# Optimization experiments

Hardware: AMD Instinct MI355X
Metric: run time of the kernel (lower is better)

The kernel has to match this reference:

```python
import jax, jax.numpy as jnp
import numpy as np

K_CONST = 0.005
D_U = 0.001
D_V = 0.005
LAYERS = [3, 256, 256, 256, 256, 2]
N_PTS = 131072


def setup_inputs() -> dict:
    key = jax.random.key(0)
    ks = jax.random.split(key, 3 + 2 * (len(LAYERS) - 1))
    inp = {
        "t": jax.random.uniform(ks[0], (N_PTS, 1), dtype=jnp.float32),
        "x": jax.random.uniform(ks[1], (N_PTS, 1), dtype=jnp.float32),
        "y": jax.random.uniform(ks[2], (N_PTS, 1), dtype=jnp.float32),
    }
    # PyTorch nn.Linear default init: U(-1/sqrt(fan_in), 1/sqrt(fan_in))
    for i in range(len(LAYERS) - 1):
        fan_in = LAYERS[i]
        s = 1.0 / np.sqrt(fan_in)
        inp[f"W{i}"] = jax.random.uniform(ks[3 + 2 * i], (LAYERS[i], LAYERS[i + 1]),
                                          minval=-s, maxval=s, dtype=jnp.float32)
        inp[f"b{i}"] = jax.random.uniform(ks[4 + 2 * i], (LAYERS[i + 1],),
                                          minval=-s, maxval=s, dtype=jnp.float32)
    return inp


def _mlp(params, inp):
    # inp: (3,) -> (2,) tanh MLP (tanh on all but last layer)
    h = inp
    for W, b in params[:-1]:
        h = jnp.tanh(h @ W + b)
    W, b = params[-1]
    return h @ W + b


def reference(t, x, y, W0, b0, W1, b1, W2, b2, W3, b3, W4, b4):
    params = [(W0, b0), (W1, b1), (W2, b2), (W3, b3), (W4, b4)]
    net = lambda p: _mlp(params, p)  # (3,) -> (2,)

    pts = jnp.concatenate([t, x, y], axis=1)            # (N, 3)
    uv = jax.vmap(net)(pts)                              # (N, 2)
    jac = jax.vmap(jax.jacrev(net))(pts)                 # (N, 2, 3)
    hess = jax.vmap(jax.jacfwd(jax.jacrev(net)))(pts)    # (N, 2, 3, 3)

    u = uv[:, 0:1]
    v = uv[:, 1:2]
    u_t = jac[:, 0, 0:1]
    v_t = jac[:, 1, 0:1]
    u_xx = hess[:, 0, 1, 1][:, None]
    u_yy = hess[:, 0, 2, 2][:, None]
    v_xx = hess[:, 1, 1, 1][:, None]
    v_yy = hess[:, 1, 2, 2][:, None]

    f = u - u ** 3 - K_CONST - v + D_U * (u_xx + u_yy) - u_t
    g = u - v + D_V * (v_xx + v_yy) - v_t
    return (u, v, f, g)
```

## Files before the change

kernel.cpp:

```cpp
#include <hip/hip_runtime.h>
#include <math.h>

#define N_PTS   131072
#define K_CONST 0.005f
#define D_U     0.001f
#define D_V     0.005f

typedef unsigned short u16;
typedef unsigned int   u32;
typedef __attribute__((ext_vector_type(8))) _Float16 f16x8;
typedef __attribute__((ext_vector_type(4))) float    f32x4;
typedef __attribute__((ext_vector_type(4))) u16      u16x4;
typedef __attribute__((ext_vector_type(8))) u16      u16x8;
typedef __attribute__((ext_vector_type(2))) u32      u32x2;
typedef __attribute__((ext_vector_type(4))) u32      u32x4;

__device__ __forceinline__ u16 f2h(float x){
    _Float16 h = (_Float16)x;
    return __builtin_bit_cast(u16, h);
}
__device__ __forceinline__ float h2f(u16 h){
    return (float)__builtin_bit_cast(_Float16, h);
}
__device__ __forceinline__ u32 pkrtz(float a, float b){
    return __builtin_bit_cast(u32, __builtin_amdgcn_cvt_pkrtz(a, b));
}
__device__ __forceinline__ u32x2 pk4(float a, float b, float c, float d){
    u32x2 r; r.x = pkrtz(a, b); r.y = pkrtz(c, d); return r;
}
__device__ __forceinline__ u32x4 pk8(const float* v){
    u32x4 r;
    r.x = pkrtz(v[0], v[1]); r.y = pkrtz(v[2], v[3]);
    r.z = pkrtz(v[4], v[5]); r.w = pkrtz(v[6], v[7]);
    return r;
}
__device__ __forceinline__ float tanh_fast(float z){
    float e = __expf(2.f * z);
    return 1.f - 2.f * __builtin_amdgcn_rcpf(e + 1.f);
}

__global__ void prep_weights(const float* __restrict__ W1, const float* __restrict__ W2,
                             const float* __restrict__ W3, u16* __restrict__ ws)
{
    int gid  = blockIdx.x * 256 + threadIdx.x;
    int lane = gid & 63;
    int nt   = (gid >> 6) & 15;
    int ks   = (gid >> 10) & 7;
    int L    = gid >> 13;
    if (L >= 3) return;
    const float* W = (L == 0) ? W1 : ((L == 1) ? W2 : W3);
    int n  = nt * 16 + (lane & 15);
    int kg = lane >> 4;
    u16 h[8];
    #pragma unroll
    for (int j = 0; j < 8; ++j) {
        int k = ks * 32 + kg * 8 + j;
        h[j] = f2h(W[k * 256 + n]);
    }
    size_t ostore = ((size_t)((L * 16 + nt) * 8 + ks) * 64 + lane) * 8;
    *(u16x8*)&ws[ostore] = *(u16x8*)h;
}


#define KSTEP(KS, WC, WN, PN, O)                                                           \
  {                                                                                        \
    WN[0] = *(const f16x8*)((PN) + 0 * 4096 + (O));                                        \
    WN[1] = *(const f16x8*)((PN) + 1 * 4096 + (O));                                        \
    WN[2] = *(const f16x8*)((PN) + 2 * 4096 + (O));                                        \
    WN[3] = *(const f16x8*)((PN) + 3 * 4096 + (O));                                        \
    int hoff = mbase + ((64 * (KS) + 16 * kg) ^ mxor);                                     \
    f16x8 hv = *(const f16x8*)(Hb + 0 * 8192 + hoff);                                      \
    f16x8 ht = *(const f16x8*)(Hb + 1 * 8192 + hoff);                                      \
    f16x8 hx = *(const f16x8*)(Hb + 2 * 8192 + hoff);                                      \
    f16x8 hy = *(const f16x8*)(Hb + 3 * 8192 + hoff);                                      \
    f16x8 hl = *(const f16x8*)(Hb + 4 * 8192 + hoff);                                      \
    _Pragma("unroll")                                                                      \
    for (int nt = 0; nt < 4; ++nt) {                                                       \
      acc[0][nt] = __builtin_amdgcn_mfma_f32_16x16x32_f16(WC[nt], hv, acc[0][nt], 0, 0, 0);\
      acc[1][nt] = __builtin_amdgcn_mfma_f32_16x16x32_f16(WC[nt], ht, acc[1][nt], 0, 0, 0);\
      acc[2][nt] = __builtin_amdgcn_mfma_f32_16x16x32_f16(WC[nt], hx, acc[2][nt], 0, 0, 0);\
      acc[3][nt] = __builtin_amdgcn_mfma_f32_16x16x32_f16(WC[nt], hy, acc[3][nt], 0, 0, 0);\
      acc[4][nt] = __builtin_amdgcn_mfma_f32_16x16x32_f16(WC[nt], hl, acc[4][nt], 0, 0, 0);\
    }                                                                                      \
  }

#define KSTEP7(WC)                                                                         \
  {                                                                                        \
    int hoff = mbase + ((64 * 7 + 16 * kg) ^ mxor);                                        \
    f16x8 hv = *(const f16x8*)(Hb + 0 * 8192 + hoff);                                      \
    f16x8 ht = *(const f16x8*)(Hb + 1 * 8192 + hoff);                                      \
    f16x8 hx = *(const f16x8*)(Hb + 2 * 8192 + hoff);                                      \
    f16x8 hy = *(const f16x8*)(Hb + 3 * 8192 + hoff);                                      \
    f16x8 hl = *(const f16x8*)(Hb + 4 * 8192 + hoff);                                      \
    _Pragma("unroll")                                                                      \
    for (int nt = 0; nt < 4; ++nt) {                                                       \
      acc[0][nt] = __builtin_amdgcn_mfma_f32_16x16x32_f16(WC[nt], hv, acc[0][nt], 0, 0, 0);\
      acc[1][nt] = __builtin_amdgcn_mfma_f32_16x16x32_f16(WC[nt], ht, acc[1][nt], 0, 0, 0);\
      acc[2][nt] = __builtin_amdgcn_mfma_f32_16x16x32_f16(WC[nt], hx, acc[2][nt], 0, 0, 0);\
      acc[3][nt] = __builtin_amdgcn_mfma_f32_16x16x32_f16(WC[nt], hy, acc[3][nt], 0, 0, 0);\
      acc[4][nt] = __builtin_amdgcn_mfma_f32_16x16x32_f16(WC[nt], hl, acc[4][nt], 0, 0, 0);\
    }                                                                                      \
  }

__global__ __launch_bounds__(256, 3)
void pinn_mfma10(const float* __restrict__ t_in, const float* __restrict__ x_in,
                 const float* __restrict__ y_in,
                 const float* __restrict__ W0, const float* __restrict__ b0,
                 const float* __restrict__ b1, const float* __restrict__ b2,
                 const float* __restrict__ b3,
                 const float* __restrict__ W4, const float* __restrict__ b4,
                 const u16* __restrict__ ws,
                 float* __restrict__ out)
{
    __shared__ u16 H[5 * 16 * 256];
    char* Hb = (char*)H;

    const int tid  = threadIdx.x;
    const int lane = tid & 63;
    const int wv   = tid >> 6;

    {
        int p = tid & 15, c = tid >> 4;
        int g0 = blockIdx.x * 16 + p;
        float tv = t_in[g0], xv = x_in[g0], yv = y_in[g0];
        #pragma unroll
        for (int half = 0; half < 2; ++half) {
            int n0 = c * 16 + half * 8;
            float w0[8], w1[8], w2[8], bb[8];
            #pragma unroll
            for (int q = 0; q < 2; ++q) {
                *(float4*)&w0[q*4] = *(const float4*)&W0[0*256 + n0 + q*4];
                *(float4*)&w1[q*4] = *(const float4*)&W0[1*256 + n0 + q*4];
                *(float4*)&w2[q*4] = *(const float4*)&W0[2*256 + n0 + q*4];
                *(float4*)&bb[q*4] = *(const float4*)&b0[n0 + q*4];
            }
            float sv[8], st[8], sx[8], sy[8], sl[8];
            #pragma unroll
            for (int j = 0; j < 8; ++j) {
                float z = tv*w0[j] + xv*w1[j] + yv*w2[j] + bb[j];
                float a = tanh_fast(z);
                float g = 1.f - a*a;
                sv[j] = a;
                st[j] = g * w0[j];
                sx[j] = g * w1[j];
                sy[j] = g * w2[j];
                sl[j] = -2.f * a * g * (w1[j]*w1[j] + w2[j]*w2[j]);
            }
            int off = p * 512 + ((2 * n0) ^ (p << 4));
            *(u32x4*)(Hb + 0*8192 + off) = pk8(sv);
            *(u32x4*)(Hb + 1*8192 + off) = pk8(st);
            *(u32x4*)(Hb + 2*8192 + off) = pk8(sx);
            *(u32x4*)(Hb + 3*8192 + off) = pk8(sy);
            *(u32x4*)(Hb + 4*8192 + off) = pk8(sl);
        }
    }
    __syncthreads();

    const int mrow  = lane & 15;
    const int kg    = lane >> 4;
    const int mxor  = mrow << 4;
    const int mbase = mrow * 512;

    const u16* pWb = ws + (size_t)(wv * 4) * 4096 + lane * 8;

    f16x8 whA[4], whB[4];
    #pragma unroll
    for (int nt = 0; nt < 4; ++nt)
        whA[nt] = *(const f16x8*)(pWb + nt * 4096);

    #pragma unroll 1
    for (int L = 0; L < 3; ++L) {
        const float* bL = (L == 0) ? b1 : ((L == 1) ? b2 : b3);

        f32x4 acc[5][4];
        #pragma unroll
        for (int s = 0; s < 5; ++s)
            #pragma unroll
            for (int nt = 0; nt < 4; ++nt)
                acc[s][nt] = (f32x4){0.f, 0.f, 0.f, 0.f};

        const u16* pL = pWb + L * 65536;
        const int  Ln = (L < 2) ? (L + 1) : 2;
        const u16* pN = pWb + Ln * 65536;

        KSTEP(0, whA, whB, pL, 1*512);
        KSTEP(1, whB, whA, pL, 2*512);
        KSTEP(2, whA, whB, pL, 3*512);
        KSTEP(3, whB, whA, pL, 4*512);
        KSTEP(4, whA, whB, pL, 5*512);
        KSTEP(5, whB, whA, pL, 6*512);
        KSTEP(6, whA, whB, pL, 7*512);
        KSTEP7(whB);

        #pragma unroll
        for (int nt = 0; nt < 4; ++nt)
            whA[nt] = *(const f16x8*)(pN + nt * 4096);

        __syncthreads();

        #pragma unroll
        for (int nt = 0; nt < 4; ++nt) {
            int nb = (wv * 4 + nt) * 16 + kg * 4;
            float4 bv = *(const float4*)&bL[nb];
            float bva[4] = {bv.x, bv.y, bv.z, bv.w};
            float oa[4], ot[4], ox[4], oy[4], ol[4];
            #pragma unroll
            for (int r = 0; r < 4; ++r) {
                float z0 = acc[0][nt][r] + bva[r];
                float a  = tanh_fast(z0);
                float g  = 1.f - a * a;
                float zt = acc[1][nt][r];
                float zx = acc[2][nt][r];
                float zy = acc[3][nt][r];
                float zl = acc[4][nt][r];
                oa[r] = a;
                ot[r] = g * zt;
                ox[r] = g * zx;
                oy[r] = g * zy;
                ol[r] = g * zl - 2.f * a * g * (zx*zx + zy*zy);
            }
            int off = mbase + ((2 * nb) ^ mxor);
            *(u32x2*)(Hb + 0*8192 + off) = pk4(oa[0], oa[1], oa[2], oa[3]);
            *(u32x2*)(Hb + 1*8192 + off) = pk4(ot[0], ot[1], ot[2], ot[3]);
            *(u32x2*)(Hb + 2*8192 + off) = pk4(ox[0], ox[1], ox[2], ox[3]);
            *(u32x2*)(Hb + 3*8192 + off) = pk4(oy[0], oy[1], oy[2], oy[3]);
            *(u32x2*)(Hb + 4*8192 + off) = pk4(ol[0], ol[1], ol[2], ol[3]);
        }
        __syncthreads();
    }

    {
        int p = tid >> 4, i = tid & 15;
        float pu = 0.f, pv = 0.f, put = 0.f, pvt = 0.f, plu = 0.f, plv = 0.f;
        #pragma unroll
        for (int half = 0; half < 2; ++half) {
            int k0  = i * 16 + half * 8;
            int off = p * 512 + ((2 * k0) ^ (p << 4));
            u16x8 hv = *(const u16x8*)(Hb + 0*8192 + off);
            u16x8 ht = *(const u16x8*)(Hb + 1*8192 + off);
            u16x8 hl = *(const u16x8*)(Hb + 4*8192 + off);
            float w4[16];
            #pragma unroll
            for (int q = 0; q < 4; ++q)
                *(float4*)&w4[q*4] = *(const float4*)&W4[k0 * 2 + q * 4];
            #pragma unroll
            for (int j = 0; j < 8; ++j) {
                float vv = h2f(hv[j]);
                float tt = h2f(ht[j]);
                float ll = h2f(hl[j]);
                float wa = w4[2*j], wb2 = w4[2*j + 1];
                pu  += vv * wa;  pv  += vv * wb2;
                put += tt * wa;  pvt += tt * wb2;
                plu += ll * wa;  plv += ll * wb2;
            }
        }
        #pragma unroll
        for (int m = 1; m < 16; m <<= 1) {
            pu  += __shfl_xor(pu, m);   pv  += __shfl_xor(pv, m);
            put += __shfl_xor(put, m);  pvt += __shfl_xor(pvt, m);
            plu += __shfl_xor(plu, m);  plv += __shfl_xor(plv, m);
        }
        if (i == 0) {
            float u = pu + b4[0];
            float v = pv + b4[1];
            int gpt = blockIdx.x * 16 + p;
            float fo = u - u*u*u - K_CONST - v + D_U * plu - put;
            float go = u - v + D_V * plv - pvt;
            out[0 * N_PTS + gpt] = u;
            out[1 * N_PTS + gpt] = v;
            out[2 * N_PTS + gpt] = fo;
            out[3 * N_PTS + gpt] = go;
        }
    }
}

#define PTS   16
#define NTHR  256
#define HDIM  256
#define KC    32
#define HPAD  260

__global__ __launch_bounds__(NTHR, 1)
void pinn_diffreact_f32(const float* __restrict__ t_in, const float* __restrict__ x_in,
                        const float* __restrict__ y_in,
                        const float* __restrict__ W0, const float* __restrict__ b0,
                        const float* __restrict__ W1, const float* __restrict__ b1,
                        const float* __restrict__ W2, const float* __restrict__ b2,
                        const float* __restrict__ W3, const float* __restrict__ b3,
                        const float* __restrict__ W4, const float* __restrict__ b4,
                        float* __restrict__ out)
{
    __shared__ float Hs[6 * PTS * HPAD];
    __shared__ float Wc[KC * HDIM];
    const int tid = threadIdx.x;
    const int pt = tid >> 4;
    const int fbase = (tid & 15) * 4;
    const int gpt = blockIdx.x * PTS + pt;
    {
        const float tv = t_in[gpt], xv = x_in[gpt], yv = y_in[gpt];
        #pragma unroll
        for (int jv = 0; jv < 4; ++jv)
            #pragma unroll
            for (int q = 0; q < 4; ++q) {
                const int f = fbase + jv * 64 + q;
                const float w0 = W0[f], w1 = W0[256 + f], w2 = W0[512 + f];
                const float z = tv*w0 + xv*w1 + yv*w2 + b0[f];
                const float a = tanhf(z), g = 1.f - a*a;
                Hs[(0*PTS+pt)*HPAD+f] = a;
                Hs[(1*PTS+pt)*HPAD+f] = g*w0;
                Hs[(2*PTS+pt)*HPAD+f] = g*w1;
                Hs[(3*PTS+pt)*HPAD+f] = g*w2;
                Hs[(4*PTS+pt)*HPAD+f] = -2.f*a*g*w1*w1;
                Hs[(5*PTS+pt)*HPAD+f] = -2.f*a*g*w2*w2;
            }
    }
    __syncthreads();
    const float* Ws[3] = {W1, W2, W3};
    const float* bs[3] = {b1, b2, b3};
    for (int L = 0; L < 3; ++L) {
        const float* __restrict__ W = Ws[L];
        const float* __restrict__ b = bs[L];
        float acc[6][16];
        #pragma unroll
        for (int s = 0; s < 6; ++s)
            #pragma unroll
            for (int j = 0; j < 16; ++j) acc[s][j] = 0.f;
        for (int kc = 0; kc < HDIM / KC; ++kc) {
            __syncthreads();
            const float4* src = (const float4*)(W + kc * KC * HDIM);
            float4* dst = (float4*)Wc;
            #pragma unroll
            for (int i2 = 0; i2 < (KC * HDIM / 4) / NTHR; ++i2)
                dst[tid + i2 * NTHR] = src[tid + i2 * NTHR];
            __syncthreads();
            #pragma unroll
            for (int k4 = 0; k4 < KC; k4 += 4) {
                float4 h[6];
                #pragma unroll
                for (int s = 0; s < 6; ++s)
                    h[s] = *(const float4*)&Hs[(s*PTS+pt)*HPAD + kc*KC + k4];
                #pragma unroll
                for (int q = 0; q < 4; ++q) {
                    float hv[6];
                    #pragma unroll
                    for (int s = 0; s < 6; ++s)
                        hv[s] = (q==0) ? h[s].x : (q==1) ? h[s].y : (q==2) ? h[s].z : h[s].w;
                    #pragma unroll
                    for (int jv = 0; jv < 4; ++jv) {
                        const float4 wq = *(const float4*)&Wc[(k4+q)*HDIM + fbase + jv*64];
                        const float wvv[4] = {wq.x, wq.y, wq.z, wq.w};
                        #pragma unroll
                        for (int r = 0; r < 4; ++r)
                            #pragma unroll
                            for (int s = 0; s < 6; ++s)
                                acc[s][jv*4+r] += hv[s] * wvv[r];
                    }
                }
            }
        }
        __syncthreads();
        #pragma unroll
        for (int jv = 0; jv < 4; ++jv)
            #pragma unroll
            for (int q = 0; q < 4; ++q) {
                const int j = jv*4+q, f = fbase + jv*64 + q;
                const float z = acc[0][j] + b[f];
                const float a = tanhf(z), g = 1.f - a*a;
                const float zt = acc[1][j], zx = acc[2][j], zy = acc[3][j];
                const float zxx = acc[4][j], zyy = acc[5][j];
                Hs[(0*PTS+pt)*HPAD+f] = a;
                Hs[(1*PTS+pt)*HPAD+f] = g*zt;
                Hs[(2*PTS+pt)*HPAD+f] = g*zx;
                Hs[(3*PTS+pt)*HPAD+f] = g*zy;
                Hs[(4*PTS+pt)*HPAD+f] = g*zxx - 2.f*a*g*zx*zx;
                Hs[(5*PTS+pt)*HPAD+f] = g*zyy - 2.f*a*g*zy*zy;
            }
        __syncthreads();
    }
    float p[6][2];
    #pragma unroll
    for (int s = 0; s < 6; ++s) { p[s][0] = 0.f; p[s][1] = 0.f; }
    #pragma unroll
    for (int jv = 0; jv < 4; ++jv)
        #pragma unroll
        for (int q = 0; q < 4; ++q) {
            const int f = fbase + jv*64 + q;
            const float w0 = W4[f*2], w1 = W4[f*2+1];
            #pragma unroll
            for (int s = 0; s < 6; ++s) {
                const float hv = Hs[(s*PTS+pt)*HPAD+f];
                p[s][0] += hv*w0; p[s][1] += hv*w1;
            }
        }
    #pragma unroll
    for (int m = 1; m < 16; m <<= 1)
        #pragma unroll
        for (int s = 0; s < 6; ++s) {
            p[s][0] += __shfl_xor(p[s][0], m);
            p[s][1] += __shfl_xor(p[s][1], m);
        }
    if ((tid & 15) == 0) {
        const float u = p[0][0] + b4[0];
        const float v = p[0][1] + b4[1];
        const float ut = p[1][0], vt = p[1][1];
        const float uxx = p[4][0], vxx = p[4][1];
        const float uyy = p[5][0], vyy = p[5][1];
        const float fo = u - u*u*u - K_CONST - v + D_U*(uxx+uyy) - ut;
        const float go = u - v + D_V*(vxx+vyy) - vt;
        out[0*N_PTS+gpt] = u;
        out[1*N_PTS+gpt] = v;
        out[2*N_PTS+gpt] = fo;
        out[3*N_PTS+gpt] = go;
    }
}

extern "C" void kernel_launch(void* const* d_in, const int* in_sizes, int n_in,
                              void* d_out, int out_size, void* d_ws, size_t ws_size,
                              hipStream_t stream)
{
    const float* t_in = (const float*)d_in[0];
    const float* x_in = (const float*)d_in[1];
    const float* y_in = (const float*)d_in[2];
    const float* W0 = (const float*)d_in[3];
    const float* b0 = (const float*)d_in[4];
    const float* W1 = (const float*)d_in[5];
    const float* b1 = (const float*)d_in[6];
    const float* W2 = (const float*)d_in[7];
    const float* b2 = (const float*)d_in[8];
    const float* W3 = (const float*)d_in[9];
    const float* b3 = (const float*)d_in[10];
    const float* W4 = (const float*)d_in[11];
    const float* b4 = (const float*)d_in[12];
    float* out = (float*)d_out;

    const size_t WS_NEEDED = (size_t)3 * 16 * 8 * 64 * 8 * 2;
    if (ws_size >= WS_NEEDED) {
        u16* ws = (u16*)d_ws;
        hipLaunchKernelGGL(prep_weights, dim3(96), dim3(256), 0, stream, W1, W2, W3, ws);
        hipLaunchKernelGGL(pinn_mfma10, dim3(N_PTS / 16), dim3(256), 0, stream,
                           t_in, x_in, y_in, W0, b0, b1, b2, b3, W4, b4, ws, out);
    } else {
        hipLaunchKernelGGL(pinn_diffreact_f32, dim3(N_PTS / PTS), dim3(NTHR), 0, stream,
                           t_in, x_in, y_in, W0, b0, W1, b1, W2, b2, W3, b3, W4, b4, out);
    }
}
```

Before: 297.5 us.

## Double-buffer LDS activations to drop mid-layer barrier and reorder weight layout

The shared activation buffer is split into two ping-pong halves, so each layer reads from one and writes the other. This removes the barrier between the MFMA reads and the epilogue writes. The prepped weight layout is also reordered so each k-step's loads for a wave are contiguous (gid-linear), simplifying the address math. The cost is double the LDS per block (80KB), and launch bounds drop from 3 to 2 blocks per CU, which reduces occupancy.

```diff
diff --git a/kernel.cpp b/kernel.cpp
--- a/kernel.cpp
+++ b/kernel.cpp
@@ -57,23 +57,22 @@
         int k = ks * 32 + kg * 8 + j;
         h[j] = f2h(W[k * 256 + n]);
     }
-    size_t ostore = ((size_t)((L * 16 + nt) * 8 + ks) * 64 + lane) * 8;
-    *(u16x8*)&ws[ostore] = *(u16x8*)h;
-}
-
-
-#define KSTEP(KS, WC, WN, PN, O)                                                           \
+    *(u16x8*)&ws[(size_t)gid * 8] = *(u16x8*)h;
+}
+
+
+#define KSTEP(KS, WC, WN, PN, RB)                                                          \
   {                                                                                        \
-    WN[0] = *(const f16x8*)((PN) + 0 * 4096 + (O));                                        \
-    WN[1] = *(const f16x8*)((PN) + 1 * 4096 + (O));                                        \
-    WN[2] = *(const f16x8*)((PN) + 2 * 4096 + (O));                                        \
-    WN[3] = *(const f16x8*)((PN) + 3 * 4096 + (O));                                        \
+    WN[0] = *(const f16x8*)((PN) + 0 * 512);                                               \
+    WN[1] = *(const f16x8*)((PN) + 1 * 512);                                               \
+    WN[2] = *(const f16x8*)((PN) + 2 * 512);                                               \
+    WN[3] = *(const f16x8*)((PN) + 3 * 512);                                               \
     int hoff = mbase + ((64 * (KS) + 16 * kg) ^ mxor);                                     \
-    f16x8 hv = *(const f16x8*)(Hb + 0 * 8192 + hoff);                                      \
-    f16x8 ht = *(const f16x8*)(Hb + 1 * 8192 + hoff);                                      \
-    f16x8 hx = *(const f16x8*)(Hb + 2 * 8192 + hoff);                                      \
-    f16x8 hy = *(const f16x8*)(Hb + 3 * 8192 + hoff);                                      \
-    f16x8 hl = *(const f16x8*)(Hb + 4 * 8192 + hoff);                                      \
+    f16x8 hv = *(const f16x8*)((RB) + 0 * 8192 + hoff);                                    \
+    f16x8 ht = *(const f16x8*)((RB) + 1 * 8192 + hoff);                                    \
+    f16x8 hx = *(const f16x8*)((RB) + 2 * 8192 + hoff);                                    \
+    f16x8 hy = *(const f16x8*)((RB) + 3 * 8192 + hoff);                                    \
+    f16x8 hl = *(const f16x8*)((RB) + 4 * 8192 + hoff);                                    \
     _Pragma("unroll")                                                                      \
     for (int nt = 0; nt < 4; ++nt) {                                                       \
       acc[0][nt] = __builtin_amdgcn_mfma_f32_16x16x32_f16(WC[nt], hv, acc[0][nt], 0, 0, 0);\
@@ -84,14 +83,14 @@
     }                                                                                      \
   }
 
-#define KSTEP7(WC)                                                                         \
+#define KSTEP7(WC, RB)                                                                     \
   {                                                                                        \
     int hoff = mbase + ((64 * 7 + 16 * kg) ^ mxor);                                        \
-    f16x8 hv = *(const f16x8*)(Hb + 0 * 8192 + hoff);                                      \
-    f16x8 ht = *(const f16x8*)(Hb + 1 * 8192 + hoff);                                      \
-    f16x8 hx = *(const f16x8*)(Hb + 2 * 8192 + hoff);                                      \
-    f16x8 hy = *(const f16x8*)(Hb + 3 * 8192 + hoff);                                      \
-    f16x8 hl = *(const f16x8*)(Hb + 4 * 8192 + hoff);                                      \
+    f16x8 hv = *(const f16x8*)((RB) + 0 * 8192 + hoff);                                    \
+    f16x8 ht = *(const f16x8*)((RB) + 1 * 8192 + hoff);                                    \
+    f16x8 hx = *(const f16x8*)((RB) + 2 * 8192 + hoff);                                    \
+    f16x8 hy = *(const f16x8*)((RB) + 3 * 8192 + hoff);                                    \
+    f16x8 hl = *(const f16x8*)((RB) + 4 * 8192 + hoff);                                    \
     _Pragma("unroll")                                                                      \
     for (int nt = 0; nt < 4; ++nt) {                                                       \
       acc[0][nt] = __builtin_amdgcn_mfma_f32_16x16x32_f16(WC[nt], hv, acc[0][nt], 0, 0, 0);\
@@ -102,8 +101,8 @@
     }                                                                                      \
   }
 
-__global__ __launch_bounds__(256, 3)
-void pinn_mfma10(const float* __restrict__ t_in, const float* __restrict__ x_in,
+__global__ __launch_bounds__(256, 2)
+void pinn_mfma13(const float* __restrict__ t_in, const float* __restrict__ x_in,
                  const float* __restrict__ y_in,
                  const float* __restrict__ W0, const float* __restrict__ b0,
                  const float* __restrict__ b1, const float* __restrict__ b2,
@@ -112,8 +111,9 @@
                  const u16* __restrict__ ws,
                  float* __restrict__ out)
 {
-    __shared__ u16 H[5 * 16 * 256];
-    char* Hb = (char*)H;
+    __shared__ u16 H[2 * 5 * 16 * 256];
+    char* Hb0 = (char*)H;
+    char* Hb1 = (char*)H + 40960;
 
     const int tid  = threadIdx.x;
     const int lane = tid & 63;
@@ -147,11 +147,11 @@
                 sl[j] = -2.f * a * g * (w1[j]*w1[j] + w2[j]*w2[j]);
             }
             int off = p * 512 + ((2 * n0) ^ (p << 4));
-            *(u32x4*)(Hb + 0*8192 + off) = pk8(sv);
-            *(u32x4*)(Hb + 1*8192 + off) = pk8(st);
-            *(u32x4*)(Hb + 2*8192 + off) = pk8(sx);
-            *(u32x4*)(Hb + 3*8192 + off) = pk8(sy);
-            *(u32x4*)(Hb + 4*8192 + off) = pk8(sl);
+            *(u32x4*)(Hb0 + 0*8192 + off) = pk8(sv);
+            *(u32x4*)(Hb0 + 1*8192 + off) = pk8(st);
+            *(u32x4*)(Hb0 + 2*8192 + off) = pk8(sx);
+            *(u32x4*)(Hb0 + 3*8192 + off) = pk8(sy);
+            *(u32x4*)(Hb0 + 4*8192 + off) = pk8(sl);
         }
     }
     __syncthreads();
@@ -161,16 +161,18 @@
     const int mxor  = mrow << 4;
     const int mbase = mrow * 512;
 
-    const u16* pWb = ws + (size_t)(wv * 4) * 4096 + lane * 8;
+    const u16* pWb = ws + wv * 2048 + lane * 8;
 
     f16x8 whA[4], whB[4];
     #pragma unroll
     for (int nt = 0; nt < 4; ++nt)
-        whA[nt] = *(const f16x8*)(pWb + nt * 4096);
+        whA[nt] = *(const f16x8*)(pWb + nt * 512);
 
     #pragma unroll 1
     for (int L = 0; L < 3; ++L) {
         const float* bL = (L == 0) ? b1 : ((L == 1) ? b2 : b3);
+        char* rbuf = (L & 1) ? Hb1 : Hb0;
+        char* wbuf = (L & 1) ? Hb0 : Hb1;
 
         f32x4 acc[5][4];
         #pragma unroll
@@ -183,20 +185,18 @@
         const int  Ln = (L < 2) ? (L + 1) : 2;
         const u16* pN = pWb + Ln * 65536;
 
-        KSTEP(0, whA, whB, pL, 1*512);
-        KSTEP(1, whB, whA, pL, 2*512);
-        KSTEP(2, whA, whB, pL, 3*512);
-        KSTEP(3, whB, whA, pL, 4*512);
-        KSTEP(4, whA, whB, pL, 5*512);
-        KSTEP(5, whB, whA, pL, 6*512);
-        KSTEP(6, whA, whB, pL, 7*512);
-        KSTEP7(whB);
+        KSTEP(0, whA, whB, pL + 1*8192, rbuf);
+        KSTEP(1, whB, whA, pL + 2*8192, rbuf);
+        KSTEP(2, whA, whB, pL + 3*8192, rbuf);
+        KSTEP(3, whB, whA, pL + 4*8192, rbuf);
+        KSTEP(4, whA, whB, pL + 5*8192, rbuf);
+        KSTEP(5, whB, whA, pL + 6*8192, rbuf);
+        KSTEP(6, whA, whB, pL + 7*8192, rbuf);
+        KSTEP7(whB, rbuf);
 
         #pragma unroll
         for (int nt = 0; nt < 4; ++nt)
-            whA[nt] = *(const f16x8*)(pN + nt * 4096);
-
-        __syncthreads();
+            whA[nt] = *(const f16x8*)(pN + nt * 512);
 
         #pragma unroll
         for (int nt = 0; nt < 4; ++nt) {
@@ -220,11 +220,11 @@
                 ol[r] = g * zl - 2.f * a * g * (zx*zx + zy*zy);
             }
             int off = mbase + ((2 * nb) ^ mxor);
-            *(u32x2*)(Hb + 0*8192 + off) = pk4(oa[0], oa[1], oa[2], oa[3]);
-            *(u32x2*)(Hb + 1*8192 + off) = pk4(ot[0], ot[1], ot[2], ot[3]);
-            *(u32x2*)(Hb + 2*8192 + off) = pk4(ox[0], ox[1], ox[2], ox[3]);
-            *(u32x2*)(Hb + 3*8192 + off) = pk4(oy[0], oy[1], oy[2], oy[3]);
-            *(u32x2*)(Hb + 4*8192 + off) = pk4(ol[0], ol[1], ol[2], ol[3]);
+            *(u32x2*)(wbuf + 0*8192 + off) = pk4(oa[0], oa[1], oa[2], oa[3]);
+            *(u32x2*)(wbuf + 1*8192 + off) = pk4(ot[0], ot[1], ot[2], ot[3]);
+            *(u32x2*)(wbuf + 2*8192 + off) = pk4(ox[0], ox[1], ox[2], ox[3]);
+            *(u32x2*)(wbuf + 3*8192 + off) = pk4(oy[0], oy[1], oy[2], oy[3]);
+            *(u32x2*)(wbuf + 4*8192 + off) = pk4(ol[0], ol[1], ol[2], ol[3]);
         }
         __syncthreads();
     }
@@ -236,9 +236,9 @@
         for (int half = 0; half < 2; ++half) {
             int k0  = i * 16 + half * 8;
             int off = p * 512 + ((2 * k0) ^ (p << 4));
-            u16x8 hv = *(const u16x8*)(Hb + 0*8192 + off);
-            u16x8 ht = *(const u16x8*)(Hb + 1*8192 + off);
-            u16x8 hl = *(const u16x8*)(Hb + 4*8192 + off);
+            u16x8 hv = *(const u16x8*)(Hb1 + 0*8192 + off);
+            u16x8 ht = *(const u16x8*)(Hb1 + 1*8192 + off);
+            u16x8 hl = *(const u16x8*)(Hb1 + 4*8192 + off);
             float w4[16];
             #pragma unroll
             for (int q = 0; q < 4; ++q)
@@ -433,11 +433,11 @@
     const float* b4 = (const float*)d_in[12];
     float* out = (float*)d_out;
 
-    const size_t WS_NEEDED = (size_t)3 * 16 * 8 * 64 * 8 * 2;
+    const size_t WS_NEEDED = (size_t)3 * 8 * 16 * 64 * 8 * 2;
     if (ws_size >= WS_NEEDED) {
         u16* ws = (u16*)d_ws;
         hipLaunchKernelGGL(prep_weights, dim3(96), dim3(256), 0, stream, W1, W2, W3, ws);
-        hipLaunchKernelGGL(pinn_mfma10, dim3(N_PTS / 16), dim3(256), 0, stream,
+        hipLaunchKernelGGL(pinn_mfma13, dim3(N_PTS / 16), dim3(256), 0, stream,
                            t_in, x_in, y_in, W0, b0, b1, b2, b3, W4, b4, ws, out);
     } else {
         hipLaunchKernelGGL(pinn_diffreact_f32, dim3(N_PTS / PTS), dim3(NTHR), 0, stream,
```

New measurement: 296.8 us. About the same (-0.2%).
